# Kernel optimization log

Measured on AMD Instinct MI355X. Metric: run time of the kernel, lower is better.

Reference implementation:

```python
import jax, jax.numpy as jnp
import numpy as np

N_NODES = 50000
N_EDGES = 800000
N_GRAPHS = 512
HIDDEN = 256
NODE_FEAT = 9
LAYERS = 4


def setup_inputs() -> dict:
    key = jax.random.key(0)
    ks = jax.random.split(key, 9)
    x = jax.random.normal(ks[0], (N_NODES, NODE_FEAT), dtype=jnp.float32)
    edge_index = jax.random.randint(ks[1], (2, N_EDGES), 0, N_NODES, dtype=jnp.int64)
    batch = jnp.sort(jax.random.randint(ks[2], (N_NODES,), 0, N_GRAPHS, dtype=jnp.int64))
    embed_W = jax.random.normal(ks[3], (NODE_FEAT, HIDDEN), dtype=jnp.float32) * (1.0 / np.sqrt(NODE_FEAT))
    embed_b = jnp.zeros((HIDDEN,), dtype=jnp.float32)
    conv_W = jax.random.normal(ks[4], (LAYERS, HIDDEN, HIDDEN), dtype=jnp.float32) * (1.0 / np.sqrt(HIDDEN))
    conv_b = jnp.zeros((LAYERS, HIDDEN), dtype=jnp.float32)
    out_W = jax.random.normal(ks[5], (HIDDEN, 1), dtype=jnp.float32) * (1.0 / np.sqrt(HIDDEN))
    out_b = jnp.zeros((1,), dtype=jnp.float32)
    return {"x": x, "edge_index": edge_index, "batch": batch,
            "embed_W": embed_W, "embed_b": embed_b,
            "conv_W": conv_W, "conv_b": conv_b,
            "out_W": out_W, "out_b": out_b}


def reference(x, edge_index, batch, embed_W, embed_b, conv_W, conv_b, out_W, out_b):
    n = x.shape[0]
    src, dst = edge_index[0], edge_index[1]
    # GCN symmetric normalization with self-loops: deg includes the self-loop (+1)
    deg = jax.ops.segment_sum(jnp.ones(src.shape[0], x.dtype), dst, num_segments=n) + 1.0
    dinv = jax.lax.rsqrt(deg)                       # [N]
    norm_e = dinv[src] * dinv[dst]                  # [E] edge coefficient
    self_coef = (dinv * dinv)[:, None]              # [N,1] self-loop coefficient

    h = jax.nn.relu(x @ embed_W + embed_b)          # [N,H]
    for l in range(conv_W.shape[0]):
        hw = h @ conv_W[l]                          # [N,H] transform first
        msg = hw[src] * norm_e[:, None]             # [E,H] gather + scale
        agg = jax.ops.segment_sum(msg, dst, num_segments=n)  # scatter-add
        agg = agg + hw * self_coef                  # self-loop contribution
        h = jax.nn.relu(agg + conv_b[l])

    # global mean pool over graph ids
    sums = jax.ops.segment_sum(h, batch, num_segments=N_GRAPHS)           # [G,H]
    cnt = jax.ops.segment_sum(jnp.ones(n, h.dtype), batch, num_segments=N_GRAPHS)
    pooled = sums / jnp.maximum(cnt, 1.0)[:, None]
    return pooled @ out_W + out_b                   # [G,1]
```

## Files before the change

### kernel.cpp

```cpp
#include <hip/hip_runtime.h>

#define N_NODES 50000
#define N_EDGES 800000
#define N_GRAPHS 512
#define HIDDEN 256
#define NODE_FEAT 9
#define LAYERS 4
#define BUCKET 64

typedef float floatx4 __attribute__((ext_vector_type(4)));
typedef short short8 __attribute__((ext_vector_type(8)));

__device__ __forceinline__ float bf2f(unsigned u) {
    unsigned v = u << 16;
    float f;
    __builtin_memcpy(&f, &v, 4);
    return f;
}
__device__ __forceinline__ unsigned short f2bf(float f) {
    unsigned v;
    __builtin_memcpy(&v, &f, 4);
    v += 0x7FFFu + ((v >> 16) & 1u);
    return (unsigned short)(v >> 16);
}

__global__ void fillb_kernel(const int* __restrict__ src, const int* __restrict__ dst,
                             int* __restrict__ cnt, int* __restrict__ col_src, int E) {
    int e = blockIdx.x * blockDim.x + threadIdx.x;
    if (e < E) {
        int d = dst[e];
        int pos = atomicAdd(&cnt[d], 1);
        if (pos < BUCKET) col_src[d * BUCKET + pos] = src[e];
    }
}

__global__ void dinv_kernel(const int* __restrict__ cnt, float* __restrict__ dinv, int N) {
    int i = blockIdx.x * blockDim.x + threadIdx.x;
    if (i < N) dinv[i] = rsqrtf((float)(cnt[i] + 1));
}

__global__ void findstart_kernel(const int* __restrict__ batch, int* __restrict__ gstart) {
    int g = blockIdx.x * blockDim.x + threadIdx.x;
    if (g > N_GRAPHS) return;
    if (g == N_GRAPHS) { gstart[g] = N_NODES; return; }
    int lo = 0, hi = N_NODES;
    while (lo < hi) {
        int mid = (lo + hi) >> 1;
        if (batch[mid] < g) lo = mid + 1; else hi = mid;
    }
    gstart[g] = lo;
}

__global__ __launch_bounds__(256) void packW_kernel(const float* __restrict__ W,
                                                    unsigned short* __restrict__ Wsw) {
    int idx = blockIdx.x * 256 + threadIdx.x;
    int lane = idx & 63;
    int ct   = (idx >> 6) & 15;
    int ks   = (idx >> 10) & 7;
    int l    = idx >> 13;
    int n = ct * 16 + (lane & 15);
    int kbase = ks * 32 + (lane >> 4) * 8;
    const float* Wl = W + (size_t)l * HIDDEN * HIDDEN;
    alignas(16) unsigned short tmp[8];
    #pragma unroll
    for (int j = 0; j < 8; j++)
        tmp[j] = f2bf(Wl[(size_t)(kbase + j) * HIDDEN + n]);
    *(uint4*)&Wsw[(size_t)idx * 8] = *(const uint4*)tmp;
}

__global__ __launch_bounds__(256) void embed_kernel(const float* __restrict__ x,
                                                    const float* __restrict__ W,
                                                    const float* __restrict__ b,
                                                    unsigned short* __restrict__ h) {
    int n = blockIdx.x;
    int c = threadIdx.x;
    float acc = b[c];
    #pragma unroll
    for (int k = 0; k < NODE_FEAT; k++)
        acc += x[n * NODE_FEAT + k] * W[k * HIDDEN + c];
    h[(size_t)n * HIDDEN + c] = f2bf(fmaxf(acc, 0.0f));
}

__global__ __launch_bounds__(256, 2) void gemm_mfma(const unsigned short* __restrict__ hin,
                                                    const unsigned short* __restrict__ Wsw,
                                                    unsigned short* __restrict__ hwout, int N) {
    __shared__ unsigned short As[64][264];
    int t = threadIdx.x;
    int wv = t >> 6, lane = t & 63, quad = lane >> 4, l15 = lane & 15;
    int n0 = blockIdx.x * 64;
    const uint4* h4 = (const uint4*)hin;

    uint4 av[8];
    #pragma unroll
    for (int i = 0; i < 8; i++) {
        int j = t + i * 256;
        int r = j >> 5;
        int c = j & 31;
        int n = n0 + r;
        av[i] = make_uint4(0u, 0u, 0u, 0u);
        if (n < N) av[i] = h4[(size_t)n * 32 + c];
    }
    const short8* Wl = (const short8*)Wsw;
    short8 bq[3][4];
    #pragma unroll
    for (int p = 0; p < 2; p++)
        #pragma unroll
        for (int ci = 0; ci < 4; ci++)
            bq[p][ci] = Wl[(size_t)(p * 16 + wv * 4 + ci) * 64 + lane];
    #pragma unroll
    for (int i = 0; i < 8; i++) {
        int j = t + i * 256;
        int r = j >> 5;
        int c = j & 31;
        *(uint4*)&As[r][c * 8] = av[i];
    }
    __syncthreads();

    floatx4 acc[4][4];
    #pragma unroll
    for (int i = 0; i < 4; i++)
        #pragma unroll
        for (int j = 0; j < 4; j++)
            acc[i][j] = (floatx4){0.f, 0.f, 0.f, 0.f};

    #pragma unroll
    for (int ks = 0; ks < 8; ks++) {
        if (ks < 6) {
            #pragma unroll
            for (int ci = 0; ci < 4; ci++)
                bq[(ks + 2) % 3][ci] = Wl[(size_t)((ks + 2) * 16 + wv * 4 + ci) * 64 + lane];
        }
        short8 a[4];
        #pragma unroll
        for (int rt = 0; rt < 4; rt++)
            a[rt] = *(const short8*)&As[rt * 16 + l15][ks * 32 + quad * 8];
        #pragma unroll
        for (int rt = 0; rt < 4; rt++)
            #pragma unroll
            for (int ci = 0; ci < 4; ci++)
                acc[rt][ci] = __builtin_amdgcn_mfma_f32_16x16x32_bf16(a[rt], bq[ks % 3][ci], acc[rt][ci], 0, 0, 0);
    }

    __syncthreads();
    #pragma unroll
    for (int rt = 0; rt < 4; rt++) {
        #pragma unroll
        for (int ci = 0; ci < 4; ci++) {
            int col = (wv * 4 + ci) * 16 + l15;
            int rowb = rt * 16 + quad * 4;
            #pragma unroll
            for (int reg = 0; reg < 4; reg++)
                As[rowb + reg][col] = f2bf(acc[rt][ci][reg]);
        }
    }
    __syncthreads();
    #pragma unroll
    for (int i = 0; i < 8; i++) {
        int j = t + i * 256;
        int r = j >> 5;
        int c = j & 31;
        int n = n0 + r;
        if (n < N)
            *(uint4*)&hwout[(size_t)n * HIDDEN + c * 8] = *(const uint4*)&As[r][c * 8];
    }
}

__device__ __forceinline__ void acc8(float* a, uint4 u, float nr) {
    a[0] += nr * bf2f(u.x & 0xFFFFu); a[1] += nr * bf2f(u.x >> 16);
    a[2] += nr * bf2f(u.y & 0xFFFFu); a[3] += nr * bf2f(u.y >> 16);
    a[4] += nr * bf2f(u.z & 0xFFFFu); a[5] += nr * bf2f(u.z >> 16);
    a[6] += nr * bf2f(u.w & 0xFFFFu); a[7] += nr * bf2f(u.w >> 16);
}

__global__ __launch_bounds__(256) void agg_kernel(const unsigned short* __restrict__ hw,
                                                  const int* __restrict__ cnt,
                                                  const int* __restrict__ col_src,
                                                  const float* __restrict__ dinv,
                                                  const float* __restrict__ bias,
                                                  unsigned short* __restrict__ hout) {
    __shared__ uint2 sEdge[4][2][BUCKET];
    int wv = threadIdx.x >> 6, lane = threadIdx.x & 63;
    int half = lane >> 5, q = lane & 31;
    int n = blockIdx.x * 8 + wv * 2 + half;
    if (n >= N_NODES) return;
    float dn = dinv[n];
    int deg = cnt[n]; if (deg > BUCKET) deg = BUCKET;

    if (q < deg) {
        int s = col_src[n * BUCKET + q];
        float nr = dinv[s] * dn;
        unsigned nrb; __builtin_memcpy(&nrb, &nr, 4);
        sEdge[wv][half][q] = make_uint2((unsigned)s, nrb);
    }
    if (q + 32 < deg) {
        int s = col_src[n * BUCKET + q + 32];
        float nr = dinv[s] * dn;
        unsigned nrb; __builtin_memcpy(&nrb, &nr, 4);
        sEdge[wv][half][q + 32] = make_uint2((unsigned)s, nrb);
    }

    uint4 s4 = ((const uint4*)(hw + (size_t)n * HIDDEN))[q];
    float selfc = dn * dn;
    float4 b0 = *(const float4*)&bias[8 * q];
    float4 b1 = *(const float4*)&bias[8 * q + 4];
    float a[8];
    a[0] = bf2f(s4.x & 0xFFFFu) * selfc + b0.x;
    a[1] = bf2f(s4.x >> 16)     * selfc + b0.y;
    a[2] = bf2f(s4.y & 0xFFFFu) * selfc + b0.z;
    a[3] = bf2f(s4.y >> 16)     * selfc + b0.w;
    a[4] = bf2f(s4.z & 0xFFFFu) * selfc + b1.x;
    a[5] = bf2f(s4.z >> 16)     * selfc + b1.y;
    a[6] = bf2f(s4.w & 0xFFFFu) * selfc + b1.z;
    a[7] = bf2f(s4.w >> 16)     * selfc + b1.w;

    const uint4* hw4 = (const uint4*)hw;
    int i = 0;
    for (; i + 4 <= deg; i += 4) {
        uint2 p0 = sEdge[wv][half][i];
        uint2 p1 = sEdge[wv][half][i + 1];
        uint2 p2 = sEdge[wv][half][i + 2];
        uint2 p3 = sEdge[wv][half][i + 3];
        uint4 u0 = hw4[(size_t)p0.x * 32 + q];
        uint4 u1 = hw4[(size_t)p1.x * 32 + q];
        uint4 u2 = hw4[(size_t)p2.x * 32 + q];
        uint4 u3 = hw4[(size_t)p3.x * 32 + q];
        float nr0, nr1, nr2, nr3;
        __builtin_memcpy(&nr0, &p0.y, 4);
        __builtin_memcpy(&nr1, &p1.y, 4);
        __builtin_memcpy(&nr2, &p2.y, 4);
        __builtin_memcpy(&nr3, &p3.y, 4);
        acc8(a, u0, nr0);
        acc8(a, u1, nr1);
        acc8(a, u2, nr2);
        acc8(a, u3, nr3);
    }
    for (; i < deg; i++) {
        uint2 p = sEdge[wv][half][i];
        uint4 u = hw4[(size_t)p.x * 32 + q];
        float nr; __builtin_memcpy(&nr, &p.y, 4);
        acc8(a, u, nr);
    }

    unsigned r0 = (unsigned)f2bf(fmaxf(a[0], 0.0f)) | ((unsigned)f2bf(fmaxf(a[1], 0.0f)) << 16);
    unsigned r1 = (unsigned)f2bf(fmaxf(a[2], 0.0f)) | ((unsigned)f2bf(fmaxf(a[3], 0.0f)) << 16);
    unsigned r2 = (unsigned)f2bf(fmaxf(a[4], 0.0f)) | ((unsigned)f2bf(fmaxf(a[5], 0.0f)) << 16);
    unsigned r3 = (unsigned)f2bf(fmaxf(a[6], 0.0f)) | ((unsigned)f2bf(fmaxf(a[7], 0.0f)) << 16);
    ((uint4*)(hout + (size_t)n * HIDDEN))[q] = make_uint4(r0, r1, r2, r3);
}

__global__ __launch_bounds__(256) void pool2_kernel(const unsigned short* __restrict__ h,
                                                    const int* __restrict__ gstart,
                                                    const float* __restrict__ outW,
                                                    const float* __restrict__ outb,
                                                    float* __restrict__ out) {
    __shared__ float sred[4];
    int g = blockIdx.x;
    int t = threadIdx.x;
    int s = gstart[g], e = gstart[g + 1];
    int half = t >> 7;
    int tc = t & 127;
    float w0 = outW[2 * tc], w1 = outW[2 * tc + 1];
    float acc = 0.0f;
    for (int n = s + half; n < e; n += 2) {
        unsigned u = *(const unsigned*)&h[(size_t)n * HIDDEN + 2 * tc];
        acc += w0 * bf2f(u & 0xFFFFu) + w1 * bf2f(u >> 16);
    }
    #pragma unroll
    for (int off = 32; off > 0; off >>= 1) acc += __shfl_down(acc, off, 64);
    if ((t & 63) == 0) sred[t >> 6] = acc;
    __syncthreads();
    if (t == 0) {
        float tot = sred[0] + sred[1] + sred[2] + sred[3];
        float cntf = (float)(e - s);
        out[g] = tot / fmaxf(cntf, 1.0f) + outb[0];
    }
}

extern "C" void kernel_launch(void* const* d_in, const int* in_sizes, int n_in,
                              void* d_out, int out_size, void* d_ws, size_t ws_size,
                              hipStream_t stream) {
    const float* x     = (const float*)d_in[0];
    const int*   edge  = (const int*)d_in[1];
    const int*   src   = edge;
    const int*   dst   = edge + N_EDGES;
    const int*   batch = (const int*)d_in[2];
    const float* embW  = (const float*)d_in[3];
    const float* embb  = (const float*)d_in[4];
    const float* convW = (const float*)d_in[5];
    const float* convb = (const float*)d_in[6];
    const float* outW  = (const float*)d_in[7];
    const float* outb  = (const float*)d_in[8];
    float* out = (float*)d_out;

    char* ws = (char*)d_ws;
    size_t off = 0;
    auto take = [&](size_t bytes) { char* p = ws + off; off += (bytes + 255) & ~(size_t)255; return p; };
    int*   cnt     = (int*)  take((size_t)N_NODES * 4);
    int*   col_src = (int*)  take((size_t)N_NODES * BUCKET * 4);
    float* dinv    = (float*)take((size_t)N_NODES * 4);
    int*   gstart  = (int*)  take((size_t)(N_GRAPHS + 1) * 4);
    unsigned short* Wsw = (unsigned short*)take((size_t)LAYERS * 8 * 16 * 64 * 8 * 2);
    unsigned short* h0  = (unsigned short*)take((size_t)N_NODES * HIDDEN * 2);
    unsigned short* h1  = (unsigned short*)take((size_t)N_NODES * HIDDEN * 2);

    hipMemsetAsync(cnt, 0, (size_t)N_NODES * 4, stream);

    fillb_kernel<<<(N_EDGES + 255) / 256, 256, 0, stream>>>(src, dst, cnt, col_src, N_EDGES);
    dinv_kernel<<<(N_NODES + 255) / 256, 256, 0, stream>>>(cnt, dinv, N_NODES);
    findstart_kernel<<<3, 256, 0, stream>>>(batch, gstart);

    packW_kernel<<<128, 256, 0, stream>>>(convW, Wsw);
    embed_kernel<<<N_NODES, 256, 0, stream>>>(x, embW, embb, h0);

    unsigned short* ha = h0;
    unsigned short* hb = h1;
    for (int l = 0; l < LAYERS; l++) {
        gemm_mfma<<<(N_NODES + 63) / 64, 256, 0, stream>>>(ha, Wsw + (size_t)l * 65536, hb, N_NODES);
        agg_kernel<<<(N_NODES + 7) / 8, 256, 0, stream>>>(hb, cnt, col_src, dinv, convb + (size_t)l * HIDDEN, ha);
    }

    pool2_kernel<<<N_GRAPHS, 256, 0, stream>>>(ha, gstart, outW, outb, out);
}
```

Baseline: 459.4 us.

## Fuse aggregation with next-layer GEMM and fold final layer into pooling

Each intermediate layer's neighbor aggregation now writes its 64-node tile into shared memory, and the next layer's MFMA GEMM consumes that tile in the same kernel. This removes the round trip of the activated hidden state through global memory and cuts the launch count. The last aggregation computes the output dot product per node directly and accumulates per-graph sums with atomics, followed by a tiny finalize kernel, which replaces the separate pooling pass. The cost is that each fused block now does its gather serially over 8 passes, so it has less parallelism than the old 8-node agg blocks. The per-graph float atomics also make the summation order nondeterministic.

```diff
diff --git a/kernel.cpp b/kernel.cpp
--- a/kernel.cpp
+++ b/kernel.cpp
@@ -172,12 +172,150 @@
     a[6] += nr * bf2f(u.w & 0xFFFFu); a[7] += nr * bf2f(u.w >> 16);
 }
 
-__global__ __launch_bounds__(256) void agg_kernel(const unsigned short* __restrict__ hw,
-                                                  const int* __restrict__ cnt,
-                                                  const int* __restrict__ col_src,
-                                                  const float* __restrict__ dinv,
-                                                  const float* __restrict__ bias,
-                                                  unsigned short* __restrict__ hout) {
+__global__ __launch_bounds__(256) void fused_agg_gemm(
+        const unsigned short* __restrict__ hw,
+        const int* __restrict__ cnt, const int* __restrict__ col_src,
+        const float* __restrict__ dinv, const float* __restrict__ bias,
+        const unsigned short* __restrict__ Wsw,
+        unsigned short* __restrict__ hwout, int N) {
+    __shared__ unsigned short As[64][264];
+    __shared__ uint2 sEdge[4][2][BUCKET];
+    int t = threadIdx.x;
+    int wv = t >> 6, lane = t & 63, quad = lane >> 4, l15 = lane & 15;
+    int half = lane >> 5, q = lane & 31;
+    int n0 = blockIdx.x * 64;
+    const uint4* hw4 = (const uint4*)hw;
+
+    float4 b0 = *(const float4*)&bias[8 * q];
+    float4 b1 = *(const float4*)&bias[8 * q + 4];
+
+    #pragma unroll 1
+    for (int p = 0; p < 8; p++) {
+        int r = p * 8 + wv * 2 + half;
+        int n = n0 + r;
+        unsigned r0 = 0, r1 = 0, r2 = 0, r3 = 0;
+        if (n < N) {
+            float dn = dinv[n];
+            int deg = cnt[n]; if (deg > BUCKET) deg = BUCKET;
+            if (q < deg) {
+                int s = col_src[n * BUCKET + q];
+                float nr = dinv[s] * dn;
+                unsigned nrb; __builtin_memcpy(&nrb, &nr, 4);
+                sEdge[wv][half][q] = make_uint2((unsigned)s, nrb);
+            }
+            if (q + 32 < deg) {
+                int s = col_src[n * BUCKET + q + 32];
+                float nr = dinv[s] * dn;
+                unsigned nrb; __builtin_memcpy(&nrb, &nr, 4);
+                sEdge[wv][half][q + 32] = make_uint2((unsigned)s, nrb);
+            }
+            uint4 s4 = hw4[(size_t)n * 32 + q];
+            float selfc = dn * dn;
+            float a[8];
+            a[0] = bf2f(s4.x & 0xFFFFu) * selfc + b0.x;
+            a[1] = bf2f(s4.x >> 16)     * selfc + b0.y;
+            a[2] = bf2f(s4.y & 0xFFFFu) * selfc + b0.z;
+            a[3] = bf2f(s4.y >> 16)     * selfc + b0.w;
+            a[4] = bf2f(s4.z & 0xFFFFu) * selfc + b1.x;
+            a[5] = bf2f(s4.z >> 16)     * selfc + b1.y;
+            a[6] = bf2f(s4.w & 0xFFFFu) * selfc + b1.z;
+            a[7] = bf2f(s4.w >> 16)     * selfc + b1.w;
+            int i = 0;
+            for (; i + 4 <= deg; i += 4) {
+                uint2 p0 = sEdge[wv][half][i];
+                uint2 p1 = sEdge[wv][half][i + 1];
+                uint2 p2 = sEdge[wv][half][i + 2];
+                uint2 p3 = sEdge[wv][half][i + 3];
+                uint4 u0 = hw4[(size_t)p0.x * 32 + q];
+                uint4 u1 = hw4[(size_t)p1.x * 32 + q];
+                uint4 u2 = hw4[(size_t)p2.x * 32 + q];
+                uint4 u3 = hw4[(size_t)p3.x * 32 + q];
+                float nr0, nr1, nr2, nr3;
+                __builtin_memcpy(&nr0, &p0.y, 4);
+                __builtin_memcpy(&nr1, &p1.y, 4);
+                __builtin_memcpy(&nr2, &p2.y, 4);
+                __builtin_memcpy(&nr3, &p3.y, 4);
+                acc8(a, u0, nr0); acc8(a, u1, nr1);
+                acc8(a, u2, nr2); acc8(a, u3, nr3);
+            }
+            for (; i < deg; i++) {
+                uint2 pe = sEdge[wv][half][i];
+                uint4 u = hw4[(size_t)pe.x * 32 + q];
+                float nr; __builtin_memcpy(&nr, &pe.y, 4);
+                acc8(a, u, nr);
+            }
+            r0 = (unsigned)f2bf(fmaxf(a[0], 0.0f)) | ((unsigned)f2bf(fmaxf(a[1], 0.0f)) << 16);
+            r1 = (unsigned)f2bf(fmaxf(a[2], 0.0f)) | ((unsigned)f2bf(fmaxf(a[3], 0.0f)) << 16);
+            r2 = (unsigned)f2bf(fmaxf(a[4], 0.0f)) | ((unsigned)f2bf(fmaxf(a[5], 0.0f)) << 16);
+            r3 = (unsigned)f2bf(fmaxf(a[6], 0.0f)) | ((unsigned)f2bf(fmaxf(a[7], 0.0f)) << 16);
+        }
+        *(uint4*)&As[r][q * 8] = make_uint4(r0, r1, r2, r3);
+    }
+
+    const short8* Wl = (const short8*)Wsw;
+    short8 bq[3][4];
+    #pragma unroll
+    for (int p = 0; p < 2; p++)
+        #pragma unroll
+        for (int ci = 0; ci < 4; ci++)
+            bq[p][ci] = Wl[(size_t)(p * 16 + wv * 4 + ci) * 64 + lane];
+    __syncthreads();
+
+    floatx4 acc[4][4];
+    #pragma unroll
+    for (int i = 0; i < 4; i++)
+        #pragma unroll
+        for (int j = 0; j < 4; j++)
+            acc[i][j] = (floatx4){0.f, 0.f, 0.f, 0.f};
+
+    #pragma unroll
+    for (int ks = 0; ks < 8; ks++) {
+        if (ks < 6) {
+            #pragma unroll
+            for (int ci = 0; ci < 4; ci++)
+                bq[(ks + 2) % 3][ci] = Wl[(size_t)((ks + 2) * 16 + wv * 4 + ci) * 64 + lane];
+        }
+        short8 a[4];
+        #pragma unroll
+        for (int rt = 0; rt < 4; rt++)
+            a[rt] = *(const short8*)&As[rt * 16 + l15][ks * 32 + quad * 8];
+        #pragma unroll
+        for (int rt = 0; rt < 4; rt++)
+            #pragma unroll
+            for (int ci = 0; ci < 4; ci++)
+                acc[rt][ci] = __builtin_amdgcn_mfma_f32_16x16x32_bf16(a[rt], bq[ks % 3][ci], acc[rt][ci], 0, 0, 0);
+    }
+
+    __syncthreads();
+    #pragma unroll
+    for (int rt = 0; rt < 4; rt++) {
+        #pragma unroll
+        for (int ci = 0; ci < 4; ci++) {
+            int col = (wv * 4 + ci) * 16 + l15;
+            int rowb = rt * 16 + quad * 4;
+            #pragma unroll
+            for (int reg = 0; reg < 4; reg++)
+                As[rowb + reg][col] = f2bf(acc[rt][ci][reg]);
+        }
+    }
+    __syncthreads();
+    #pragma unroll
+    for (int i = 0; i < 8; i++) {
+        int j = t + i * 256;
+        int r = j >> 5;
+        int c = j & 31;
+        int n = n0 + r;
+        if (n < N)
+            *(uint4*)&hwout[(size_t)n * HIDDEN + c * 8] = *(const uint4*)&As[r][c * 8];
+    }
+}
+
+__global__ __launch_bounds__(256) void agg_pool_kernel(
+        const unsigned short* __restrict__ hw,
+        const int* __restrict__ cnt, const int* __restrict__ col_src,
+        const float* __restrict__ dinv, const float* __restrict__ bias,
+        const int* __restrict__ batch, const float* __restrict__ outW,
+        float* __restrict__ gsum) {
     __shared__ uint2 sEdge[4][2][BUCKET];
     int wv = threadIdx.x >> 6, lane = threadIdx.x & 63;
     int half = lane >> 5, q = lane & 31;
@@ -199,7 +337,8 @@
         sEdge[wv][half][q + 32] = make_uint2((unsigned)s, nrb);
     }
 
-    uint4 s4 = ((const uint4*)(hw + (size_t)n * HIDDEN))[q];
+    const uint4* hw4 = (const uint4*)hw;
+    uint4 s4 = hw4[(size_t)n * 32 + q];
     float selfc = dn * dn;
     float4 b0 = *(const float4*)&bias[8 * q];
     float4 b1 = *(const float4*)&bias[8 * q + 4];
@@ -213,7 +352,6 @@
     a[6] = bf2f(s4.w & 0xFFFFu) * selfc + b1.z;
     a[7] = bf2f(s4.w >> 16)     * selfc + b1.w;
 
-    const uint4* hw4 = (const uint4*)hw;
     int i = 0;
     for (; i + 4 <= deg; i += 4) {
         uint2 p0 = sEdge[wv][half][i];
@@ -229,50 +367,35 @@
         __builtin_memcpy(&nr1, &p1.y, 4);
         __builtin_memcpy(&nr2, &p2.y, 4);
         __builtin_memcpy(&nr3, &p3.y, 4);
-        acc8(a, u0, nr0);
-        acc8(a, u1, nr1);
-        acc8(a, u2, nr2);
-        acc8(a, u3, nr3);
+        acc8(a, u0, nr0); acc8(a, u1, nr1);
+        acc8(a, u2, nr2); acc8(a, u3, nr3);
     }
     for (; i < deg; i++) {
-        uint2 p = sEdge[wv][half][i];
-        uint4 u = hw4[(size_t)p.x * 32 + q];
-        float nr; __builtin_memcpy(&nr, &p.y, 4);
+        uint2 pe = sEdge[wv][half][i];
+        uint4 u = hw4[(size_t)pe.x * 32 + q];
+        float nr; __builtin_memcpy(&nr, &pe.y, 4);
         acc8(a, u, nr);
     }
 
-    unsigned r0 = (unsigned)f2bf(fmaxf(a[0], 0.0f)) | ((unsigned)f2bf(fmaxf(a[1], 0.0f)) << 16);
-    unsigned r1 = (unsigned)f2bf(fmaxf(a[2], 0.0f)) | ((unsigned)f2bf(fmaxf(a[3], 0.0f)) << 16);
-    unsigned r2 = (unsigned)f2bf(fmaxf(a[4], 0.0f)) | ((unsigned)f2bf(fmaxf(a[5], 0.0f)) << 16);
-    unsigned r3 = (unsigned)f2bf(fmaxf(a[6], 0.0f)) | ((unsigned)f2bf(fmaxf(a[7], 0.0f)) << 16);
-    ((uint4*)(hout + (size_t)n * HIDDEN))[q] = make_uint4(r0, r1, r2, r3);
-}
-
-__global__ __launch_bounds__(256) void pool2_kernel(const unsigned short* __restrict__ h,
-                                                    const int* __restrict__ gstart,
-                                                    const float* __restrict__ outW,
-                                                    const float* __restrict__ outb,
-                                                    float* __restrict__ out) {
-    __shared__ float sred[4];
-    int g = blockIdx.x;
-    int t = threadIdx.x;
-    int s = gstart[g], e = gstart[g + 1];
-    int half = t >> 7;
-    int tc = t & 127;
-    float w0 = outW[2 * tc], w1 = outW[2 * tc + 1];
-    float acc = 0.0f;
-    for (int n = s + half; n < e; n += 2) {
-        unsigned u = *(const unsigned*)&h[(size_t)n * HIDDEN + 2 * tc];
-        acc += w0 * bf2f(u & 0xFFFFu) + w1 * bf2f(u >> 16);
-    }
-    #pragma unroll
-    for (int off = 32; off > 0; off >>= 1) acc += __shfl_down(acc, off, 64);
-    if ((t & 63) == 0) sred[t >> 6] = acc;
-    __syncthreads();
-    if (t == 0) {
-        float tot = sred[0] + sred[1] + sred[2] + sred[3];
-        float cntf = (float)(e - s);
-        out[g] = tot / fmaxf(cntf, 1.0f) + outb[0];
+    float4 w0 = *(const float4*)&outW[8 * q];
+    float4 w1 = *(const float4*)&outW[8 * q + 4];
+    float dot = fmaxf(a[0], 0.0f) * w0.x + fmaxf(a[1], 0.0f) * w0.y
+              + fmaxf(a[2], 0.0f) * w0.z + fmaxf(a[3], 0.0f) * w0.w
+              + fmaxf(a[4], 0.0f) * w1.x + fmaxf(a[5], 0.0f) * w1.y
+              + fmaxf(a[6], 0.0f) * w1.z + fmaxf(a[7], 0.0f) * w1.w;
+    #pragma unroll
+    for (int off = 16; off > 0; off >>= 1) dot += __shfl_xor(dot, off, 64);
+    if (q == 0) atomicAdd(&gsum[batch[n]], dot);
+}
+
+__global__ void finalize_kernel(const float* __restrict__ gsum,
+                                const int* __restrict__ gstart,
+                                const float* __restrict__ outb,
+                                float* __restrict__ out) {
+    int g = blockIdx.x * blockDim.x + threadIdx.x;
+    if (g < N_GRAPHS) {
+        float c = (float)(gstart[g + 1] - gstart[g]);
+        out[g] = gsum[g] / fmaxf(c, 1.0f) + outb[0];
     }
 }
 
@@ -299,11 +422,13 @@
     int*   col_src = (int*)  take((size_t)N_NODES * BUCKET * 4);
     float* dinv    = (float*)take((size_t)N_NODES * 4);
     int*   gstart  = (int*)  take((size_t)(N_GRAPHS + 1) * 4);
+    float* gsum    = (float*)take((size_t)N_GRAPHS * 4);
     unsigned short* Wsw = (unsigned short*)take((size_t)LAYERS * 8 * 16 * 64 * 8 * 2);
     unsigned short* h0  = (unsigned short*)take((size_t)N_NODES * HIDDEN * 2);
     unsigned short* h1  = (unsigned short*)take((size_t)N_NODES * HIDDEN * 2);
 
     hipMemsetAsync(cnt, 0, (size_t)N_NODES * 4, stream);
+    hipMemsetAsync(gsum, 0, (size_t)N_GRAPHS * 4, stream);
 
     fillb_kernel<<<(N_EDGES + 255) / 256, 256, 0, stream>>>(src, dst, cnt, col_src, N_EDGES);
     dinv_kernel<<<(N_NODES + 255) / 256, 256, 0, stream>>>(cnt, dinv, N_NODES);
@@ -312,12 +437,15 @@
     packW_kernel<<<128, 256, 0, stream>>>(convW, Wsw);
     embed_kernel<<<N_NODES, 256, 0, stream>>>(x, embW, embb, h0);
 
-    unsigned short* ha = h0;
-    unsigned short* hb = h1;
-    for (int l = 0; l < LAYERS; l++) {
-        gemm_mfma<<<(N_NODES + 63) / 64, 256, 0, stream>>>(ha, Wsw + (size_t)l * 65536, hb, N_NODES);
-        agg_kernel<<<(N_NODES + 7) / 8, 256, 0, stream>>>(hb, cnt, col_src, dinv, convb + (size_t)l * HIDDEN, ha);
-    }
-
-    pool2_kernel<<<N_GRAPHS, 256, 0, stream>>>(ha, gstart, outW, outb, out);
-}
+    int nblk = (N_NODES + 63) / 64;
+    gemm_mfma<<<nblk, 256, 0, stream>>>(h0, Wsw, h1, N_NODES);
+    fused_agg_gemm<<<nblk, 256, 0, stream>>>(h1, cnt, col_src, dinv, convb + 0 * HIDDEN,
+                                             Wsw + (size_t)1 * 65536, h0, N_NODES);
+    fused_agg_gemm<<<nblk, 256, 0, stream>>>(h0, cnt, col_src, dinv, convb + 1 * HIDDEN,
+                                             Wsw + (size_t)2 * 65536, h1, N_NODES);
+    fused_agg_gemm<<<nblk, 256, 0, stream>>>(h1, cnt, col_src, dinv, convb + 2 * HIDDEN,
+                                             Wsw + (size_t)3 * 65536, h0, N_NODES);
+    agg_pool_kernel<<<(N_NODES + 7) / 8, 256, 0, stream>>>(h0, cnt, col_src, dinv,
+                                                           convb + 3 * HIDDEN, batch, outW, gsum);
+    finalize_kernel<<<2, 256, 0, stream>>>(gsum, gstart, outb, out);
+}
```

New measurement: 552.9 us. +20.3%, slower.
